# Kernel tuning notes

Measured on AMD Instinct MI355X. Metric: run time of the kernel, lower is better.

The kernel has to match this reference:

```python
import jax, jax.numpy as jnp
import numpy as np

B, S, H = 32, 1024, 512
NEG = -1e10

def setup_inputs() -> dict:
    key = jax.random.key(0)
    k1, k2, k3, k4, k5, k6 = jax.random.split(key, 6)
    return {
        "hidden": jax.random.normal(k1, (B, H), jnp.float32),
        "encoder_outputs": jax.random.normal(k2, (B, S, 2 * H), jnp.float32),
        "mask": jax.random.randint(k3, (B, S), 0, 2, jnp.int32),
        "W_attn": jax.random.normal(k4, (3 * H, H), jnp.float32) * (1.0 / np.sqrt(3 * H)),
        "b_attn": jax.random.normal(k5, (H,), jnp.float32) * 0.01,
        "W_v": jax.random.normal(k6, (H,), jnp.float32) * (1.0 / np.sqrt(H)),
    }

def reference(hidden, encoder_outputs, mask, W_attn, b_attn, W_v):
    # Split the concat-matmul: cat([h, enc]) @ W_attn == h @ W_h + enc @ W_e
    W_h, W_e = W_attn[:H], W_attn[H:]            # [H,H], [2H,H]
    proj_h = hidden @ W_h                        # [B, H]
    proj_e = jnp.einsum('bse,eh->bsh', encoder_outputs, W_e)  # [B, S, H]
    energy = jnp.tanh(proj_h[:, None, :] + proj_e + b_attn)   # [B, S, H]
    scores = jnp.einsum('bsh,h->bs', energy, W_v)             # [B, S]
    scores = jnp.where(mask == 0, NEG, scores)
    attn_w = jax.nn.softmax(scores, axis=1)                   # [B, S]
    context = jnp.einsum('bs,bse->be', attn_w, encoder_outputs)  # [B, 2H]
    return context, attn_w
```

## Files before the change

### kernel.cpp

```cpp
#include <hip/hip_runtime.h>
#include <hip/hip_bf16.h>
#include <math.h>

#define NB 32
#define NS 1024
#define NH 512
#define NE 1024
#define NEGV -1e10f

typedef _Float16 f16x8 __attribute__((ext_vector_type(8)));
typedef _Float16 f16x4 __attribute__((ext_vector_type(4)));
typedef float f32x4 __attribute__((ext_vector_type(4)));

__device__ __forceinline__ float fast_tanh(float x) {
  float t = __expf(2.f * x);
  return (t - 1.f) * __builtin_amdgcn_rcpf(t + 1.f);
}

__global__ __launch_bounds__(256) void proj_h_kernel(
    const float* __restrict__ hidden, const float* __restrict__ W_attn,
    const float* __restrict__ b_attn, float* __restrict__ c) {
  int b = blockIdx.x >> 1;
  int h = ((blockIdx.x & 1) << 8) + threadIdx.x;
  __shared__ float hid[NH];
  for (int e = threadIdx.x; e < NH; e += 256) hid[e] = hidden[b * NH + e];
  __syncthreads();
  float acc = b_attn[h];
#pragma unroll 8
  for (int e = 0; e < NH; ++e) acc = fmaf(hid[e], W_attn[(size_t)e * NH + h], acc);
  c[b * NH + h] = acc;
}

__global__ __launch_bounds__(256) void prep_We_kernel(
    const float* __restrict__ W_attn, _Float16* __restrict__ Bp) {
  int kt = blockIdx.x;
  int t = threadIdx.x;
#pragma unroll
  for (int p = 0; p < 8; ++p) {
    int f = (p << 8) + t;
    int wid = f >> 8;
    int nj = (f >> 6) & 3;
    int lane = f & 63;
    int col = (wid << 6) + (nj << 4) + (lane & 15);
    int kb = (kt << 5) + ((lane >> 4) << 3);
    f16x8 h;
#pragma unroll
    for (int j = 0; j < 8; ++j)
      h[j] = (_Float16)W_attn[(size_t)(NH + kb + j) * NH + col];
    *(f16x8*)((char*)Bp + (size_t)(((kt << 3) + wid) << 12) + (nj << 10) + (lane << 4)) = h;
  }
}

__global__ __launch_bounds__(512, 4) void score_kernel(
    const float* __restrict__ enc, const _Float16* __restrict__ Bp,
    const float* __restrict__ c, const float* __restrict__ Wv,
    float* __restrict__ spart) {
  __shared__ float Asm[2][64 * 32];
  const int tid = threadIdx.x;
  const int lane = tid & 63;
  const int wid = tid >> 6;
  const int r15 = lane & 15;
  const int id = blockIdx.x;
  const int mt = ((id & 7) << 6) + (id >> 3);
  const int b = mt >> 4;
  const int s0 = (mt & 15) << 6;
  const char* Abase = (const char*)(enc + ((size_t)b * NS + s0) * NE);
  const char* Bbase = (const char*)Bp + ((size_t)wid << 12);

  f32x4 acc[4][4];
#pragma unroll
  for (int i = 0; i < 4; ++i)
#pragma unroll
    for (int j = 0; j < 4; ++j) acc[i][j] = (f32x4)0.f;

#define STAGE_A(KT, BUF)                                                         \
  {                                                                              \
    int d = tid << 4;                                                            \
    int row = d >> 7;                                                            \
    int sb = (d & 127) ^ ((row & 7) << 4);                                       \
    __builtin_amdgcn_global_load_lds(                                            \
        (const __attribute__((address_space(1))) uint32_t*)(Abase + (size_t)row * 4096 + ((KT) << 7) + sb), \
        (__attribute__((address_space(3))) uint32_t*)((char*)Asm[BUF] + (wid << 10)), \
        16, 0, 0);                                                               \
  }

#define BLOAD(S, KT)                                                             \
  _Pragma("unroll") for (int nj = 0; nj < 4; ++nj)                               \
      bf##S[nj] = *(const f16x8*)(Bbase + ((size_t)(KT) << 15) +                 \
                                  (nj << 10) + (lane << 4));

#define COMPUTE(CUR, S)                                                          \
  {                                                                              \
    f16x8 af[4];                                                                 \
    _Pragma("unroll") for (int mi = 0; mi < 4; ++mi) {                           \
      int row = (mi << 4) + r15;                                                 \
      int off1 = (row << 7) + ((lane >> 4) << 5);                                \
      int x = (row & 7) << 4;                                                    \
      f32x4 u = *(const f32x4*)((const char*)Asm[CUR] + (off1 ^ x));             \
      f32x4 v = *(const f32x4*)((const char*)Asm[CUR] + ((off1 + 16) ^ x));      \
      f16x8 h;                                                                   \
      h[0] = (_Float16)u[0]; h[1] = (_Float16)u[1];                              \
      h[2] = (_Float16)u[2]; h[3] = (_Float16)u[3];                              \
      h[4] = (_Float16)v[0]; h[5] = (_Float16)v[1];                              \
      h[6] = (_Float16)v[2]; h[7] = (_Float16)v[3];                              \
      af[mi] = h;                                                                \
    }                                                                            \
    _Pragma("unroll") for (int mi = 0; mi < 4; ++mi)                             \
      _Pragma("unroll") for (int nj = 0; nj < 4; ++nj)                           \
        acc[mi][nj] = __builtin_amdgcn_mfma_f32_16x16x32_f16(af[mi], bf##S[nj],  \
                                                             acc[mi][nj], 0, 0, 0); \
  }

  f16x8 bf0[4], bf1[4];
  STAGE_A(0, 0);
  BLOAD(0, 0);
  __syncthreads();
  for (int kt = 0; kt < 32; kt += 2) {
    STAGE_A(kt + 1, 1);
    BLOAD(1, kt + 1);
    COMPUTE(0, 0);
    __syncthreads();
    if (kt < 30) {
      STAGE_A(kt + 2, 0);
      BLOAD(0, kt + 2);
    }
    COMPUTE(1, 1);
    __syncthreads();
  }
#undef STAGE_A
#undef BLOAD
#undef COMPUTE

  float sr[4][4];
#pragma unroll
  for (int i = 0; i < 4; ++i)
#pragma unroll
    for (int r = 0; r < 4; ++r) sr[i][r] = 0.f;
#pragma unroll
  for (int nj = 0; nj < 4; ++nj) {
    int hcol = (wid << 6) + (nj << 4) + r15;
    float wvj = Wv[hcol];
    float cvj = c[b * NH + hcol];
#pragma unroll
    for (int mi = 0; mi < 4; ++mi)
#pragma unroll
      for (int r = 0; r < 4; ++r)
        sr[mi][r] += wvj * fast_tanh(acc[mi][nj][r] + cvj);
  }
#pragma unroll
  for (int off = 1; off < 16; off <<= 1)
#pragma unroll
    for (int mi = 0; mi < 4; ++mi)
#pragma unroll
      for (int r = 0; r < 4; ++r) sr[mi][r] += __shfl_xor(sr[mi][r], off, 64);
  if (r15 == 0) {
    float* dst = spart + (size_t)wid * NB * NS + b * NS + s0;
#pragma unroll
    for (int mi = 0; mi < 4; ++mi)
#pragma unroll
      for (int r = 0; r < 4; ++r)
        dst[(mi << 4) + ((lane >> 4) << 2) + r] = sr[mi][r];
  }
}

__global__ __launch_bounds__(256) void softmax_kernel(
    const float* __restrict__ spart, const int* __restrict__ mask,
    float* __restrict__ attn) {
  int b = blockIdx.x, tid = threadIdx.x;
  __shared__ float red[8];
  float v[4];
  float mx = -INFINITY;
#pragma unroll
  for (int j = 0; j < 4; ++j) {
    int s = tid + (j << 8);
    float x = 0.f;
#pragma unroll
    for (int p = 0; p < 8; ++p) x += spart[(size_t)p * NB * NS + b * NS + s];
    v[j] = (mask[b * NS + s] == 0) ? NEGV : x;
    mx = fmaxf(mx, v[j]);
  }
#pragma unroll
  for (int off = 32; off >= 1; off >>= 1) mx = fmaxf(mx, __shfl_xor(mx, off, 64));
  if ((tid & 63) == 0) red[tid >> 6] = mx;
  __syncthreads();
  mx = fmaxf(fmaxf(red[0], red[1]), fmaxf(red[2], red[3]));
  float sum = 0.f;
#pragma unroll
  for (int j = 0; j < 4; ++j) {
    v[j] = __expf(v[j] - mx);
    sum += v[j];
  }
#pragma unroll
  for (int off = 32; off >= 1; off >>= 1) sum += __shfl_xor(sum, off, 64);
  __syncthreads();
  if ((tid & 63) == 0) red[4 + (tid >> 6)] = sum;
  __syncthreads();
  float inv = 1.f / (red[4] + red[5] + red[6] + red[7]);
#pragma unroll
  for (int j = 0; j < 4; ++j) attn[b * NS + tid + (j << 8)] = v[j] * inv;
}

__global__ __launch_bounds__(256) void ctx_partial_kernel(
    const float* __restrict__ enc, const float* __restrict__ attn,
    float* __restrict__ partial) {
  int ch = blockIdx.x;
  int b = blockIdx.y;
  int tid = threadIdx.x;
  __shared__ float w[64];
  if (tid < 64) w[tid] = attn[b * NS + (ch << 6) + tid];
  __syncthreads();
  const float* encb = enc + ((size_t)b * NS + (ch << 6)) * NE;
  float4 acc = make_float4(0.f, 0.f, 0.f, 0.f);
  int e = tid << 2;
  for (int s = 0; s < 64; ++s) {
    float4 x = *(const float4*)(encb + (size_t)s * NE + e);
    float ws_ = w[s];
    acc.x = fmaf(ws_, x.x, acc.x);
    acc.y = fmaf(ws_, x.y, acc.y);
    acc.z = fmaf(ws_, x.z, acc.z);
    acc.w = fmaf(ws_, x.w, acc.w);
  }
  *(float4*)(partial + ((size_t)(b * 16 + ch)) * NE + e) = acc;
}

__global__ __launch_bounds__(256) void ctx_reduce_kernel(
    const float* __restrict__ partial, float* __restrict__ ctx) {
  int b = blockIdx.x;
  int e = threadIdx.x << 2;
  float4 acc = make_float4(0.f, 0.f, 0.f, 0.f);
  for (int ch = 0; ch < 16; ++ch) {
    float4 x = *(const float4*)(partial + ((size_t)(b * 16 + ch)) * NE + e);
    acc.x += x.x;
    acc.y += x.y;
    acc.z += x.z;
    acc.w += x.w;
  }
  *(float4*)(ctx + (size_t)b * NE + e) = acc;
}

extern "C" void kernel_launch(void* const* d_in, const int* in_sizes, int n_in,
                              void* d_out, int out_size, void* d_ws, size_t ws_size,
                              hipStream_t stream) {
  const float* hidden = (const float*)d_in[0];
  const float* enc = (const float*)d_in[1];
  const int* mask = (const int*)d_in[2];
  const float* W_attn = (const float*)d_in[3];
  const float* b_attn = (const float*)d_in[4];
  const float* W_v = (const float*)d_in[5];

  float* ctx = (float*)d_out;
  float* attn = ctx + NB * NS;

  char* ws = (char*)d_ws;
  float* c = (float*)ws;
  float* spart = (float*)(ws + 65536);
  float* partial = (float*)(ws + 65536 + 1048576);
  _Float16* Bp = (_Float16*)(ws + 65536 + 1048576 + 2097152);

  proj_h_kernel<<<64, 256, 0, stream>>>(hidden, W_attn, b_attn, c);
  prep_We_kernel<<<32, 256, 0, stream>>>(W_attn, Bp);
  score_kernel<<<512, 512, 0, stream>>>(enc, Bp, c, W_v, spart);
  softmax_kernel<<<NB, 256, 0, stream>>>(spart, mask, attn);
  ctx_partial_kernel<<<dim3(16, NB), 256, 0, stream>>>(enc, attn, partial);
  ctx_reduce_kernel<<<NB, 256, 0, stream>>>(partial, ctx);
}
```

Baseline: 103.1 us.

## Enlarge score GEMM tile to 128 rows, reduce scores in-block, fine-grained waits

The score kernel now uses 1024-thread blocks covering 128 sequence rows with a 2x8 wave grid, so each block loads the fp16 weight tiles once for twice as many rows. The per-wave partial scores are summed in shared memory inside the block and written as final scores, which removes the 8-way spart buffer and its re-reads in softmax. The loop barriers become explicit vmcnt/lgkmcnt waits plus s_barrier so loads for the next stage can stay in flight. In exchange the grid halves to 256 blocks, which may leave CUs underfilled, and the larger blocks raise register and LDS pressure per CU.

```diff
diff --git a/kernel.cpp b/kernel.cpp
--- a/kernel.cpp
+++ b/kernel.cpp
@@ -38,34 +38,35 @@
 #pragma unroll
   for (int p = 0; p < 8; ++p) {
     int f = (p << 8) + t;
-    int wid = f >> 8;
+    int ws = f >> 8;
     int nj = (f >> 6) & 3;
     int lane = f & 63;
-    int col = (wid << 6) + (nj << 4) + (lane & 15);
+    int col = (ws << 6) + (nj << 4) + (lane & 15);
     int kb = (kt << 5) + ((lane >> 4) << 3);
     f16x8 h;
 #pragma unroll
     for (int j = 0; j < 8; ++j)
       h[j] = (_Float16)W_attn[(size_t)(NH + kb + j) * NH + col];
-    *(f16x8*)((char*)Bp + (size_t)(((kt << 3) + wid) << 12) + (nj << 10) + (lane << 4)) = h;
-  }
-}
-
-__global__ __launch_bounds__(512, 4) void score_kernel(
+    *(f16x8*)((char*)Bp + (size_t)(((kt << 3) + ws) << 12) + (nj << 10) + (lane << 4)) = h;
+  }
+}
+
+__global__ __launch_bounds__(1024) void score_kernel(
     const float* __restrict__ enc, const _Float16* __restrict__ Bp,
     const float* __restrict__ c, const float* __restrict__ Wv,
-    float* __restrict__ spart) {
-  __shared__ float Asm[2][64 * 32];
+    float* __restrict__ scores) {
+  __shared__ float Asm[2][128 * 32];
   const int tid = threadIdx.x;
   const int lane = tid & 63;
   const int wid = tid >> 6;
+  const int wr = wid >> 3;
+  const int wc = wid & 7;
   const int r15 = lane & 15;
-  const int id = blockIdx.x;
-  const int mt = ((id & 7) << 6) + (id >> 3);
-  const int b = mt >> 4;
-  const int s0 = (mt & 15) << 6;
+  const int mt = blockIdx.x;
+  const int b = mt >> 3;
+  const int s0 = (mt & 7) << 7;
   const char* Abase = (const char*)(enc + ((size_t)b * NS + s0) * NE);
-  const char* Bbase = (const char*)Bp + ((size_t)wid << 12);
+  const char* Bbase = (const char*)Bp + ((size_t)wc << 12);
 
   f32x4 acc[4][4];
 #pragma unroll
@@ -93,7 +94,7 @@
   {                                                                              \
     f16x8 af[4];                                                                 \
     _Pragma("unroll") for (int mi = 0; mi < 4; ++mi) {                           \
-      int row = (mi << 4) + r15;                                                 \
+      int row = (wr << 6) + (mi << 4) + r15;                                     \
       int off1 = (row << 7) + ((lane >> 4) << 5);                                \
       int x = (row & 7) << 4;                                                    \
       f32x4 u = *(const f32x4*)((const char*)Asm[CUR] + (off1 ^ x));             \
@@ -111,25 +112,43 @@
                                                              acc[mi][nj], 0, 0, 0); \
   }
 
+#define WAITBAR(N)                                                               \
+  asm volatile("s_waitcnt vmcnt(" #N ")" ::: "memory");                          \
+  __builtin_amdgcn_s_barrier();                                                  \
+  __builtin_amdgcn_sched_barrier(0);
+
+#define ENDBAR()                                                                 \
+  asm volatile("s_waitcnt lgkmcnt(0)" ::: "memory");                             \
+  __builtin_amdgcn_s_barrier();                                                  \
+  __builtin_amdgcn_sched_barrier(0);
+
   f16x8 bf0[4], bf1[4];
   STAGE_A(0, 0);
   BLOAD(0, 0);
-  __syncthreads();
-  for (int kt = 0; kt < 32; kt += 2) {
+  for (int kt = 0; kt < 30; kt += 2) {
     STAGE_A(kt + 1, 1);
     BLOAD(1, kt + 1);
+    WAITBAR(5)
     COMPUTE(0, 0);
-    __syncthreads();
-    if (kt < 30) {
-      STAGE_A(kt + 2, 0);
-      BLOAD(0, kt + 2);
-    }
+    ENDBAR()
+    STAGE_A(kt + 2, 0);
+    BLOAD(0, kt + 2);
+    WAITBAR(5)
     COMPUTE(1, 1);
-    __syncthreads();
-  }
+    ENDBAR()
+  }
+  STAGE_A(31, 1);
+  BLOAD(1, 31);
+  WAITBAR(5)
+  COMPUTE(0, 0);
+  ENDBAR()
+  WAITBAR(0)
+  COMPUTE(1, 1);
 #undef STAGE_A
 #undef BLOAD
 #undef COMPUTE
+#undef WAITBAR
+#undef ENDBAR
 
   float sr[4][4];
 #pragma unroll
@@ -138,7 +157,7 @@
     for (int r = 0; r < 4; ++r) sr[i][r] = 0.f;
 #pragma unroll
   for (int nj = 0; nj < 4; ++nj) {
-    int hcol = (wid << 6) + (nj << 4) + r15;
+    int hcol = (wc << 6) + (nj << 4) + r15;
     float wvj = Wv[hcol];
     float cvj = c[b * NH + hcol];
 #pragma unroll
@@ -153,18 +172,28 @@
     for (int mi = 0; mi < 4; ++mi)
 #pragma unroll
       for (int r = 0; r < 4; ++r) sr[mi][r] += __shfl_xor(sr[mi][r], off, 64);
+  __syncthreads();
+  float* red = (float*)Asm;
   if (r15 == 0) {
-    float* dst = spart + (size_t)wid * NB * NS + b * NS + s0;
 #pragma unroll
     for (int mi = 0; mi < 4; ++mi)
 #pragma unroll
-      for (int r = 0; r < 4; ++r)
-        dst[(mi << 4) + ((lane >> 4) << 2) + r] = sr[mi][r];
+      for (int r = 0; r < 4; ++r) {
+        int row = (wr << 6) + (mi << 4) + ((lane >> 4) << 2) + r;
+        red[(row << 3) + wc] = sr[mi][r];
+      }
+  }
+  __syncthreads();
+  if (tid < 128) {
+    float s = 0.f;
+#pragma unroll
+    for (int w = 0; w < 8; ++w) s += red[(tid << 3) + w];
+    scores[b * NS + s0 + tid] = s;
   }
 }
 
 __global__ __launch_bounds__(256) void softmax_kernel(
-    const float* __restrict__ spart, const int* __restrict__ mask,
+    const float* __restrict__ scores, const int* __restrict__ mask,
     float* __restrict__ attn) {
   int b = blockIdx.x, tid = threadIdx.x;
   __shared__ float red[8];
@@ -173,9 +202,7 @@
 #pragma unroll
   for (int j = 0; j < 4; ++j) {
     int s = tid + (j << 8);
-    float x = 0.f;
-#pragma unroll
-    for (int p = 0; p < 8; ++p) x += spart[(size_t)p * NB * NS + b * NS + s];
+    float x = scores[b * NS + s];
     v[j] = (mask[b * NS + s] == 0) ? NEGV : x;
     mx = fmaxf(mx, v[j]);
   }
@@ -253,14 +280,14 @@
 
   char* ws = (char*)d_ws;
   float* c = (float*)ws;
-  float* spart = (float*)(ws + 65536);
-  float* partial = (float*)(ws + 65536 + 1048576);
-  _Float16* Bp = (_Float16*)(ws + 65536 + 1048576 + 2097152);
+  float* scores = (float*)(ws + 65536);
+  float* partial = (float*)(ws + 65536 + 131072);
+  _Float16* Bp = (_Float16*)(ws + 65536 + 131072 + 2097152);
 
   proj_h_kernel<<<64, 256, 0, stream>>>(hidden, W_attn, b_attn, c);
   prep_We_kernel<<<32, 256, 0, stream>>>(W_attn, Bp);
-  score_kernel<<<512, 512, 0, stream>>>(enc, Bp, c, W_v, spart);
-  softmax_kernel<<<NB, 256, 0, stream>>>(spart, mask, attn);
+  score_kernel<<<256, 1024, 0, stream>>>(enc, Bp, c, W_v, scores);
+  softmax_kernel<<<NB, 256, 0, stream>>>(scores, mask, attn);
   ctx_partial_kernel<<<dim3(16, NB), 256, 0, stream>>>(enc, attn, partial);
   ctx_reduce_kernel<<<NB, 256, 0, stream>>>(partial, ctx);
 }
```

New measurement: 108.5 us. 1.05x slower.

## Deepen score GEMM A-tile pipeline to four LDS buffers with explicit waitcnt

Applied to the files above, without the earlier changes.

Changes the score kernel's encoder-tile staging from double buffering to a four-buffer ring with three tiles in flight. Each iteration uses explicit vmcnt/lgkmcnt waits and raw s_barrier instead of __syncthreads, so it waits only for the oldest tile. This is meant to hide more global-load latency behind MFMA work. In exchange LDS use doubles to 32KB and the occupancy hint in launch_bounds is dropped. The wrapped modulo indices issue a few redundant tail loads, and the hand-counted vmcnt must match the actual outstanding loads.

```diff
diff --git a/kernel.cpp b/kernel.cpp
--- a/kernel.cpp
+++ b/kernel.cpp
@@ -33,29 +33,29 @@
 
 __global__ __launch_bounds__(256) void prep_We_kernel(
     const float* __restrict__ W_attn, _Float16* __restrict__ Bp) {
-  int kt = blockIdx.x;
+  int ks = blockIdx.x;
   int t = threadIdx.x;
 #pragma unroll
   for (int p = 0; p < 8; ++p) {
     int f = (p << 8) + t;
-    int wid = f >> 8;
+    int ws = f >> 8;
     int nj = (f >> 6) & 3;
     int lane = f & 63;
-    int col = (wid << 6) + (nj << 4) + (lane & 15);
-    int kb = (kt << 5) + ((lane >> 4) << 3);
+    int col = (ws << 6) + (nj << 4) + (lane & 15);
+    int kb = (ks << 5) + ((lane >> 4) << 3);
     f16x8 h;
 #pragma unroll
     for (int j = 0; j < 8; ++j)
       h[j] = (_Float16)W_attn[(size_t)(NH + kb + j) * NH + col];
-    *(f16x8*)((char*)Bp + (size_t)(((kt << 3) + wid) << 12) + (nj << 10) + (lane << 4)) = h;
-  }
-}
-
-__global__ __launch_bounds__(512, 4) void score_kernel(
+    *(f16x8*)((char*)Bp + (size_t)(((ks << 3) + ws) << 12) + (nj << 10) + (lane << 4)) = h;
+  }
+}
+
+__global__ __launch_bounds__(512) void score_kernel(
     const float* __restrict__ enc, const _Float16* __restrict__ Bp,
     const float* __restrict__ c, const float* __restrict__ Wv,
     float* __restrict__ spart) {
-  __shared__ float Asm[2][64 * 32];
+  __shared__ float Asm[4][64 * 32];
   const int tid = threadIdx.x;
   const int lane = tid & 63;
   const int wid = tid >> 6;
@@ -79,25 +79,25 @@
     int row = d >> 7;                                                            \
     int sb = (d & 127) ^ ((row & 7) << 4);                                       \
     __builtin_amdgcn_global_load_lds(                                            \
-        (const __attribute__((address_space(1))) uint32_t*)(Abase + (size_t)row * 4096 + ((KT) << 7) + sb), \
-        (__attribute__((address_space(3))) uint32_t*)((char*)Asm[BUF] + (wid << 10)), \
+        (const __attribute__((address_space(1))) uint32_t*)(Abase + (size_t)row * 4096 + ((size_t)(KT) << 7) + sb), \
+        (__attribute__((address_space(3))) uint32_t*)((char*)Asm + ((BUF) << 13) + (wid << 10)), \
         16, 0, 0);                                                               \
   }
 
-#define BLOAD(S, KT)                                                             \
+#define BLOAD(ARR, KT)                                                           \
   _Pragma("unroll") for (int nj = 0; nj < 4; ++nj)                               \
-      bf##S[nj] = *(const f16x8*)(Bbase + ((size_t)(KT) << 15) +                 \
-                                  (nj << 10) + (lane << 4));
-
-#define COMPUTE(CUR, S)                                                          \
+      ARR[nj] = *(const f16x8*)(Bbase + ((size_t)(KT) << 15) +                   \
+                                (nj << 10) + (lane << 4));
+
+#define COMPUTE(BUF, ARR)                                                        \
   {                                                                              \
     f16x8 af[4];                                                                 \
     _Pragma("unroll") for (int mi = 0; mi < 4; ++mi) {                           \
       int row = (mi << 4) + r15;                                                 \
-      int off1 = (row << 7) + ((lane >> 4) << 5);                                \
+      int off1 = ((BUF) << 13) + (row << 7) + ((lane >> 4) << 5);                \
       int x = (row & 7) << 4;                                                    \
-      f32x4 u = *(const f32x4*)((const char*)Asm[CUR] + (off1 ^ x));             \
-      f32x4 v = *(const f32x4*)((const char*)Asm[CUR] + ((off1 + 16) ^ x));      \
+      f32x4 u = *(const f32x4*)((const char*)Asm + (off1 ^ x));                  \
+      f32x4 v = *(const f32x4*)((const char*)Asm + ((off1 + 16) ^ x));           \
       f16x8 h;                                                                   \
       h[0] = (_Float16)u[0]; h[1] = (_Float16)u[1];                              \
       h[2] = (_Float16)u[2]; h[3] = (_Float16)u[3];                              \
@@ -107,29 +107,36 @@
     }                                                                            \
     _Pragma("unroll") for (int mi = 0; mi < 4; ++mi)                             \
       _Pragma("unroll") for (int nj = 0; nj < 4; ++nj)                           \
-        acc[mi][nj] = __builtin_amdgcn_mfma_f32_16x16x32_f16(af[mi], bf##S[nj],  \
+        acc[mi][nj] = __builtin_amdgcn_mfma_f32_16x16x32_f16(af[mi], ARR[nj],    \
                                                              acc[mi][nj], 0, 0, 0); \
   }
+
+#define ITER(T, ABUF_T, ABUF_T3, BF_T, BF_T1)                                    \
+  STAGE_A(((T) + 3) & 31, ABUF_T3);                                              \
+  BLOAD(BF_T1, ((T) + 1) & 31);                                                  \
+  asm volatile("s_waitcnt vmcnt(5)" ::: "memory");                               \
+  __builtin_amdgcn_s_barrier();                                                  \
+  __builtin_amdgcn_sched_barrier(0);                                             \
+  COMPUTE(ABUF_T, BF_T);                                                         \
+  asm volatile("s_waitcnt lgkmcnt(0)" ::: "memory");                             \
+  __builtin_amdgcn_s_barrier();                                                  \
+  __builtin_amdgcn_sched_barrier(0);
 
   f16x8 bf0[4], bf1[4];
   STAGE_A(0, 0);
-  BLOAD(0, 0);
-  __syncthreads();
-  for (int kt = 0; kt < 32; kt += 2) {
-    STAGE_A(kt + 1, 1);
-    BLOAD(1, kt + 1);
-    COMPUTE(0, 0);
-    __syncthreads();
-    if (kt < 30) {
-      STAGE_A(kt + 2, 0);
-      BLOAD(0, kt + 2);
-    }
-    COMPUTE(1, 1);
-    __syncthreads();
+  STAGE_A(1, 1);
+  STAGE_A(2, 2);
+  BLOAD(bf0, 0);
+  for (int kt = 0; kt < 32; kt += 4) {
+    ITER(kt + 0, 0, 3, bf0, bf1)
+    ITER(kt + 1, 1, 0, bf1, bf0)
+    ITER(kt + 2, 2, 1, bf0, bf1)
+    ITER(kt + 3, 3, 2, bf1, bf0)
   }
 #undef STAGE_A
 #undef BLOAD
 #undef COMPUTE
+#undef ITER
 
   float sr[4][4];
 #pragma unroll
```

Result: slower. 116.3 us (+12.9%).
